# Kernel tuning notes

Hardware: AMD Instinct MI355X
Metric: run time of the kernel (lower is better)

Reference implementation:

```python
import jax, jax.numpy as jnp
import numpy as np

NUM_HEADS = 12
HEAD_DIM = 64
LOGIT_SCALE_MAX = 4.605170185988092  # log(1/0.01), open_clip default
EPS = 1e-12  # F.normalize eps


def setup_inputs() -> dict:
    key = jax.random.key(0)
    ks = jax.random.split(key, 8)
    N, L, C = 2, 2048, 768
    return {
        "x": jax.random.normal(ks[0], (N, L, C), dtype=jnp.float32),
        "in_proj_w": jax.random.normal(ks[1], (3 * C, C), dtype=jnp.float32) * 0.02,
        "in_proj_b": jax.random.normal(ks[2], (3 * C,), dtype=jnp.float32) * 0.02,
        "logit_scale": jax.random.normal(ks[3], (NUM_HEADS, 1, 1), dtype=jnp.float32),
        "learned_scale": jnp.ones((NUM_HEADS,), dtype=jnp.float32),
        "out_proj_w": jax.random.normal(ks[4], (C, C), dtype=jnp.float32) * 0.02,
        "out_proj_b": jax.random.normal(ks[5], (C,), dtype=jnp.float32) * 0.02,
        "attn_mask": jnp.zeros((L, L), dtype=jnp.float32),
    }


def _l2norm(t):
    # F.normalize(dim=-1): x / max(||x||, eps)
    n = jnp.linalg.norm(t, axis=-1, keepdims=True)
    return t / jnp.maximum(n, EPS)


def reference(x, in_proj_w, in_proj_b, logit_scale, learned_scale,
              out_proj_w, out_proj_b, attn_mask):
    N, L, C = x.shape
    H, D = NUM_HEADS, HEAD_DIM
    # packed QKV projection: [N, L, 3C]
    qkv = jnp.einsum("nlc,fc->nlf", x, in_proj_w) + in_proj_b
    q, k, v = jnp.split(qkv, 3, axis=-1)
    # [N, L, C] -> [N, H, L, D]
    to_heads = lambda t: t.reshape(N, L, H, D).transpose(0, 2, 1, 3)
    q, k, v = to_heads(q), to_heads(k), to_heads(v)
    # cosine attention with clamped exp logit scale per head
    attn = jnp.einsum("nhld,nhmd->nhlm", _l2norm(q), _l2norm(k))
    ls = jnp.exp(jnp.minimum(logit_scale, LOGIT_SCALE_MAX))  # [H,1,1]
    attn = attn * ls[None]  # broadcast over [N,H,L,L]
    attn = attn + attn_mask  # additive mask [L,L]
    attn = jax.nn.softmax(attn, axis=-1)
    out = jnp.einsum("nhlm,nhmd->nhld", attn, v)
    # learned per-head output scale
    out = out * learned_scale[None, :, None, None]
    # [N,H,L,D] -> [N,L,C]
    out = out.transpose(0, 2, 1, 3).reshape(N, L, C)
    out = jnp.einsum("nlc,fc->nlf", out, out_proj_w) + out_proj_b
    return out
```

## Files before the change

kernel.cpp:

```cpp
#include <hip/hip_runtime.h>
#include <math.h>

#define NB   2
#define SEQ  2048
#define CH   768
#define NH   12
#define HD   64
#define F3   2304
#define LSMAX 4.605170185988092f
#define LOG2E 1.4426950408889634f

typedef _Float16 f16;
typedef __attribute__((ext_vector_type(8))) _Float16 f16x8;
typedef __attribute__((ext_vector_type(4))) _Float16 f16x4;
typedef __attribute__((ext_vector_type(2))) _Float16 f16x2;
typedef __attribute__((ext_vector_type(4))) float f32x4;

#define QSZ   3145728
#define OATT  (3 * QSZ)
#define XHOFF 12582912
#define W1OFF 15728640
#define W2OFF 17498112
#define FLAGO 18087936

#define KP   72
#define VP   136
#define PPIT 76
#define GP   40

__global__ __launch_bounds__(256) void cvt_f16(const float* __restrict__ X,
                                               const float* __restrict__ W1,
                                               const float* __restrict__ W2,
                                               const float* __restrict__ M,
                                               f16* __restrict__ Xh,
                                               f16* __restrict__ W1h,
                                               f16* __restrict__ W2h,
                                               int* __restrict__ flag)
{
    int tid = blockIdx.x * 256 + threadIdx.x;
    if (blockIdx.y == 3) {
        if (tid < 1048576) {
            float4 v = ((const float4*)M)[tid];
            bool nz = (v.x != 0.f) || (v.y != 0.f) || (v.z != 0.f) || (v.w != 0.f);
            if (__any(nz) && (threadIdx.x & 63) == 0) atomicOr(flag, 1);
        }
        return;
    }
    const float* src; f16* dst; int n4;
    switch (blockIdx.y) {
        case 0:  src = X;  dst = Xh;  n4 = 786432;  break;
        case 1:  src = W1; dst = W1h; n4 = 442368;  break;
        default: src = W2; dst = W2h; n4 = 147456;  break;
    }
    if (tid < n4) {
        float4 v = ((const float4*)src)[tid];
        f16x4 o = {(f16)v.x, (f16)v.y, (f16)v.z, (f16)v.w};
        ((f16x4*)dst)[tid] = o;
    }
}

__global__ __launch_bounds__(256, 3) void qkv_gemm(const f16* __restrict__ Xh,
                                                   const f16* __restrict__ Wh,
                                                   const float* __restrict__ bias,
                                                   const float* __restrict__ logit_scale,
                                                   f16* __restrict__ qkv16)
{
    __shared__ f16 As[128 * GP];
    __shared__ f16 Bs[128 * GP];
    const int t    = threadIdx.x;
    const int w    = t >> 6;
    const int lane = t & 63;
    const int quad = lane >> 4;
    const int sub  = lane & 15;
    const int wm   = w & 1, wn = w >> 1;
    const int f0   = blockIdx.x * 128;
    const int m0   = blockIdx.y * 128;
    const int srow = t >> 1;
    const int sk   = (t & 1) * 16;

    const f16* ag = Xh + (size_t)(m0 + srow) * CH + sk;
    const f16* bg = Wh + (size_t)(f0 + srow) * CH + sk;
    f16x8 a0 = *(const f16x8*)(ag);
    f16x8 a1 = *(const f16x8*)(ag + 8);
    f16x8 b0 = *(const f16x8*)(bg);
    f16x8 b1 = *(const f16x8*)(bg + 8);

    f32x4 acc[4][4];
#pragma unroll
    for (int i = 0; i < 4; ++i)
#pragma unroll
        for (int j = 0; j < 4; ++j) acc[i][j] = (f32x4){0.f, 0.f, 0.f, 0.f};

    for (int k0 = 0; k0 < CH; k0 += 32) {
        __syncthreads();
        *(f16x8*)&As[srow * GP + sk + 0] = a0;
        *(f16x8*)&As[srow * GP + sk + 8] = a1;
        *(f16x8*)&Bs[srow * GP + sk + 0] = b0;
        *(f16x8*)&Bs[srow * GP + sk + 8] = b1;
        __syncthreads();
        if (k0 + 32 < CH) {
            a0 = *(const f16x8*)(ag + k0 + 32);
            a1 = *(const f16x8*)(ag + k0 + 40);
            b0 = *(const f16x8*)(bg + k0 + 32);
            b1 = *(const f16x8*)(bg + k0 + 40);
        }
        f16x8 af[4], bf[4];
#pragma unroll
        for (int i = 0; i < 4; ++i) {
            af[i] = *(const f16x8*)&As[(wm * 64 + i * 16 + sub) * GP + quad * 8];
            bf[i] = *(const f16x8*)&Bs[(wn * 64 + i * 16 + sub) * GP + quad * 8];
        }
#pragma unroll
        for (int i = 0; i < 4; ++i)
#pragma unroll
            for (int j = 0; j < 4; ++j)
                acc[i][j] = __builtin_amdgcn_mfma_f32_16x16x32_f16(af[i], bf[j], acc[i][j], 0, 0, 0);
    }

    const int t3 = f0 / CH;
    const int h  = ((f0 + wn * 64) % CH) >> 6;
    f16* dst = qkv16 + (size_t)t3 * QSZ;
    float lsv = (t3 == 0) ? __expf(fminf(logit_scale[h], LSMAX)) * LOG2E : 1.0f;
    float bb[4];
#pragma unroll
    for (int j = 0; j < 4; ++j) bb[j] = bias[f0 + wn * 64 + j * 16 + sub];
#pragma unroll
    for (int i = 0; i < 4; ++i) {
#pragma unroll
        for (int r = 0; r < 4; ++r) {
            int m = m0 + wm * 64 + i * 16 + quad * 4 + r;
            int n = m >> 11, l = m & 2047;
            float v[4];
#pragma unroll
            for (int j = 0; j < 4; ++j) v[j] = acc[i][j][r] + bb[j];
            float scale = 1.0f;
            if (t3 < 2) {
                float ss = v[0] * v[0] + v[1] * v[1] + v[2] * v[2] + v[3] * v[3];
#pragma unroll
                for (int mk = 1; mk < 16; mk <<= 1) ss += __shfl_xor(ss, mk, 64);
                scale = 1.0f / fmaxf(sqrtf(ss), 1e-12f);
                if (t3 == 0) scale *= lsv;
            }
            f16* drow = dst + (((size_t)n * NH + h) * SEQ + l) * HD;
#pragma unroll
            for (int j = 0; j < 4; ++j)
                drow[j * 16 + sub] = (f16)(v[j] * scale);
        }
    }
}

__global__ __launch_bounds__(256, 3) void attn(const f16* __restrict__ Qh,
                                               const f16* __restrict__ Kh,
                                               const f16* __restrict__ Vh,
                                               const float* __restrict__ M32,
                                               const float* __restrict__ lscale,
                                               const int* __restrict__ flag,
                                               f16* __restrict__ Og)
{
    __shared__ f16 Ks[128 * KP];
    __shared__ f16 Vt[64 * VP];
    __shared__ f16 QP[64 * PPIT];

    const int t    = threadIdx.x;
    const int w    = t >> 6;
    const int lane = t & 63;
    const int quad = lane >> 4;
    const int sub  = lane & 15;
    const int qb   = blockIdx.x * 64;
    const int h    = blockIdx.y, n = blockIdx.z;
    const bool has_mask = (*flag) != 0;

    const f16* Qg = Qh + ((size_t)(n * NH + h) * SEQ + qb) * HD;
    const f16* Kg = Kh + (size_t)(n * NH + h) * SEQ * HD;
    const f16* Vg = Vh + (size_t)(n * NH + h) * SEQ * HD;
    const float* Mg = M32 + (size_t)(qb + w * 16 + quad * 4) * SEQ;

#pragma unroll
    for (int rep = 0; rep < 2; ++rep) {
        int id = rep * 256 + t;
        int row = id >> 3, c8 = id & 7;
        f16x8 v = *(const f16x8*)&Qg[row * 64 + c8 * 8];
        *(f16x4*)&QP[row * PPIT + c8 * 8 + 0] = (f16x4){v[0], v[1], v[2], v[3]};
        *(f16x4*)&QP[row * PPIT + c8 * 8 + 4] = (f16x4){v[4], v[5], v[6], v[7]};
    }

    const int krow = t >> 1;
    const int kcb  = (t & 1) * 32;
    f16x8 kr0, kr1, kr2, kr3, vr0, vr1, vr2, vr3;
    {
        const f16* kp = Kg + krow * 64 + kcb;
        kr0 = *(const f16x8*)(kp + 0);
        kr1 = *(const f16x8*)(kp + 8);
        kr2 = *(const f16x8*)(kp + 16);
        kr3 = *(const f16x8*)(kp + 24);
        const f16* vp = Vg + (2 * lane) * 64 + w * 16;
        vr0 = *(const f16x8*)(vp + 0);
        vr1 = *(const f16x8*)(vp + 8);
        vr2 = *(const f16x8*)(vp + 64);
        vr3 = *(const f16x8*)(vp + 72);
    }

    __syncthreads();
    f16x8 qf0, qf1;
    {
        f16x4 l0 = *(const f16x4*)&QP[(w * 16 + sub) * PPIT + quad * 8];
        f16x4 l1 = *(const f16x4*)&QP[(w * 16 + sub) * PPIT + quad * 8 + 4];
        f16x4 l2 = *(const f16x4*)&QP[(w * 16 + sub) * PPIT + 32 + quad * 8];
        f16x4 l3 = *(const f16x4*)&QP[(w * 16 + sub) * PPIT + 32 + quad * 8 + 4];
        qf0 = (f16x8){l0[0], l0[1], l0[2], l0[3], l1[0], l1[1], l1[2], l1[3]};
        qf1 = (f16x8){l2[0], l2[1], l2[2], l2[3], l3[0], l3[1], l3[2], l3[3]};
    }

    {
        f16* kd = &Ks[krow * KP + kcb];
        *(f16x8*)(kd + 0)  = kr0;
        *(f16x8*)(kd + 8)  = kr1;
        *(f16x8*)(kd + 16) = kr2;
        *(f16x8*)(kd + 24) = kr3;
#pragma unroll
        for (int j = 0; j < 8; ++j) {
            *(f16x2*)&Vt[(w * 16 + j) * VP + 2 * lane]     = (f16x2){vr0[j], vr2[j]};
            *(f16x2*)&Vt[(w * 16 + 8 + j) * VP + 2 * lane] = (f16x2){vr1[j], vr3[j]};
        }
    }
    __syncthreads();

    const f16x8 ones = {(f16)1.f, (f16)1.f, (f16)1.f, (f16)1.f,
                        (f16)1.f, (f16)1.f, (f16)1.f, (f16)1.f};
    f32x4 o[4];
    f32x4 l_acc = (f32x4){0.f, 0.f, 0.f, 0.f};
    float m_run[4];
#pragma unroll
    for (int dt = 0; dt < 4; ++dt) o[dt] = (f32x4){0.f, 0.f, 0.f, 0.f};
#pragma unroll
    for (int r = 0; r < 4; ++r) m_run[r] = -1e30f;

    const int NITER = SEQ / 128;
    for (int c = 0; c < NITER; ++c) {
        const int c0 = c * 128;
        if (c + 1 < NITER) {
            const f16* kp = Kg + (c0 + 128 + krow) * 64 + kcb;
            kr0 = *(const f16x8*)(kp + 0);
            kr1 = *(const f16x8*)(kp + 8);
            kr2 = *(const f16x8*)(kp + 16);
            kr3 = *(const f16x8*)(kp + 24);
            const f16* vp = Vg + (c0 + 128 + 2 * lane) * 64 + w * 16;
            vr0 = *(const f16x8*)(vp + 0);
            vr1 = *(const f16x8*)(vp + 8);
            vr2 = *(const f16x8*)(vp + 64);
            vr3 = *(const f16x8*)(vp + 72);
        }

        f32x4 s[8];
#pragma unroll
        for (int ct = 0; ct < 8; ++ct) {
            f16x8 kf0 = *(const f16x8*)&Ks[(ct * 16 + sub) * KP + quad * 8];
            f16x8 kf1 = *(const f16x8*)&Ks[(ct * 16 + sub) * KP + 32 + quad * 8];
            f32x4 a = (f32x4){0.f, 0.f, 0.f, 0.f};
            a = __builtin_amdgcn_mfma_f32_16x16x32_f16(qf0, kf0, a, 0, 0, 0);
            a = __builtin_amdgcn_mfma_f32_16x16x32_f16(qf1, kf1, a, 0, 0, 0);
            s[ct] = a;
        }
        if (has_mask) {
#pragma unroll
            for (int ct = 0; ct < 8; ++ct)
#pragma unroll
                for (int r = 0; r < 4; ++r)
                    s[ct][r] += LOG2E * Mg[(size_t)r * SEQ + c0 + ct * 16 + sub];
        }
        float mnew[4];
#pragma unroll
        for (int r = 0; r < 4; ++r) {
            float a01 = fmaxf(s[0][r], s[1][r]), a23 = fmaxf(s[2][r], s[3][r]);
            float a45 = fmaxf(s[4][r], s[5][r]), a67 = fmaxf(s[6][r], s[7][r]);
            mnew[r] = fmaxf(fmaxf(fmaxf(a01, a23), fmaxf(a45, a67)), m_run[r]);
        }
        {
            union { f16x2 h; int i; } p0, p1, v0, v1;
            p0.h = (f16x2){(f16)mnew[0], (f16)mnew[1]};
            p1.h = (f16x2){(f16)mnew[2], (f16)mnew[3]};
#pragma unroll
            for (int mk = 1; mk < 16; mk <<= 1) {
                v0.i = __shfl_xor(p0.i, mk, 64);
                v1.i = __shfl_xor(p1.i, mk, 64);
                p0.h = __builtin_elementwise_max(p0.h, v0.h);
                p1.h = __builtin_elementwise_max(p1.h, v1.h);
            }
            mnew[0] = (float)p0.h[0]; mnew[1] = (float)p0.h[1];
            mnew[2] = (float)p1.h[0]; mnew[3] = (float)p1.h[1];
        }
        float alpha[4];
#pragma unroll
        for (int r = 0; r < 4; ++r) {
            alpha[r] = exp2f(m_run[r] - mnew[r]);
            m_run[r] = mnew[r];
        }
#pragma unroll
        for (int dt = 0; dt < 4; ++dt)
#pragma unroll
            for (int r = 0; r < 4; ++r) o[dt][r] *= alpha[r];
#pragma unroll
        for (int r = 0; r < 4; ++r) l_acc[r] *= alpha[r];

#pragma unroll
        for (int hf = 0; hf < 2; ++hf) {
#pragma unroll
            for (int ct = 0; ct < 4; ++ct)
#pragma unroll
                for (int r = 0; r < 4; ++r) {
                    float p = exp2f(s[hf * 4 + ct][r] - mnew[r]);
                    QP[(w * 16 + quad * 4 + r) * PPIT + ct * 16 + sub] = (f16)p;
                }
            f16x4 p00 = *(const f16x4*)&QP[(w * 16 + sub) * PPIT + quad * 8];
            f16x4 p01 = *(const f16x4*)&QP[(w * 16 + sub) * PPIT + quad * 8 + 4];
            f16x4 p10 = *(const f16x4*)&QP[(w * 16 + sub) * PPIT + 32 + quad * 8];
            f16x4 p11 = *(const f16x4*)&QP[(w * 16 + sub) * PPIT + 32 + quad * 8 + 4];
            f16x8 pf0 = {p00[0], p00[1], p00[2], p00[3], p01[0], p01[1], p01[2], p01[3]};
            f16x8 pf1 = {p10[0], p10[1], p10[2], p10[3], p11[0], p11[1], p11[2], p11[3]};
            l_acc = __builtin_amdgcn_mfma_f32_16x16x32_f16(pf0, ones, l_acc, 0, 0, 0);
            l_acc = __builtin_amdgcn_mfma_f32_16x16x32_f16(pf1, ones, l_acc, 0, 0, 0);
#pragma unroll
            for (int dt = 0; dt < 4; ++dt) {
                f16x8 vf0 = *(const f16x8*)&Vt[(dt * 16 + sub) * VP + hf * 64 + quad * 8];
                f16x8 vf1 = *(const f16x8*)&Vt[(dt * 16 + sub) * VP + hf * 64 + 32 + quad * 8];
                o[dt] = __builtin_amdgcn_mfma_f32_16x16x32_f16(pf0, vf0, o[dt], 0, 0, 0);
                o[dt] = __builtin_amdgcn_mfma_f32_16x16x32_f16(pf1, vf1, o[dt], 0, 0, 0);
            }
        }

        if (c + 1 < NITER) {
            __syncthreads();
            f16* kd = &Ks[krow * KP + kcb];
            *(f16x8*)(kd + 0)  = kr0;
            *(f16x8*)(kd + 8)  = kr1;
            *(f16x8*)(kd + 16) = kr2;
            *(f16x8*)(kd + 24) = kr3;
#pragma unroll
            for (int j = 0; j < 8; ++j) {
                *(f16x2*)&Vt[(w * 16 + j) * VP + 2 * lane]     = (f16x2){vr0[j], vr2[j]};
                *(f16x2*)&Vt[(w * 16 + 8 + j) * VP + 2 * lane] = (f16x2){vr1[j], vr3[j]};
            }
            __syncthreads();
        }
    }
    float lsc = lscale[h];
#pragma unroll
    for (int r = 0; r < 4; ++r) {
        float inv = lsc / l_acc[r];
        int q = qb + w * 16 + quad * 4 + r;
#pragma unroll
        for (int dt = 0; dt < 4; ++dt)
            Og[((size_t)n * SEQ + q) * CH + h * 64 + dt * 16 + sub] =
                (f16)(o[dt][r] * inv);
    }
}

__global__ __launch_bounds__(256, 3) void out_gemm(const f16* __restrict__ A,
                                                   const f16* __restrict__ Wh,
                                                   const float* __restrict__ bias,
                                                   float* __restrict__ out)
{
    __shared__ f16 As[128 * GP];
    __shared__ f16 Bs[128 * GP];
    const int t    = threadIdx.x;
    const int w    = t >> 6;
    const int lane = t & 63;
    const int quad = lane >> 4;
    const int sub  = lane & 15;
    const int wm   = w & 1, wn = w >> 1;
    const int f0   = blockIdx.x * 128;
    const int m0   = blockIdx.y * 128;
    const int srow = t >> 1;
    const int sk   = (t & 1) * 16;

    const f16* ag = A + (size_t)(m0 + srow) * CH + sk;
    const f16* bg = Wh + (size_t)(f0 + srow) * CH + sk;
    f16x8 a0 = *(const f16x8*)(ag);
    f16x8 a1 = *(const f16x8*)(ag + 8);
    f16x8 b0 = *(const f16x8*)(bg);
    f16x8 b1 = *(const f16x8*)(bg + 8);

    f32x4 acc[4][4];
#pragma unroll
    for (int i = 0; i < 4; ++i)
#pragma unroll
        for (int j = 0; j < 4; ++j) acc[i][j] = (f32x4){0.f, 0.f, 0.f, 0.f};

    for (int k0 = 0; k0 < CH; k0 += 32) {
        __syncthreads();
        *(f16x8*)&As[srow * GP + sk + 0] = a0;
        *(f16x8*)&As[srow * GP + sk + 8] = a1;
        *(f16x8*)&Bs[srow * GP + sk + 0] = b0;
        *(f16x8*)&Bs[srow * GP + sk + 8] = b1;
        __syncthreads();
        if (k0 + 32 < CH) {
            a0 = *(const f16x8*)(ag + k0 + 32);
            a1 = *(const f16x8*)(ag + k0 + 40);
            b0 = *(const f16x8*)(bg + k0 + 32);
            b1 = *(const f16x8*)(bg + k0 + 40);
        }
        f16x8 af[4], bf[4];
#pragma unroll
        for (int i = 0; i < 4; ++i) {
            af[i] = *(const f16x8*)&As[(wm * 64 + i * 16 + sub) * GP + quad * 8];
            bf[i] = *(const f16x8*)&Bs[(wn * 64 + i * 16 + sub) * GP + quad * 8];
        }
#pragma unroll
        for (int i = 0; i < 4; ++i)
#pragma unroll
            for (int j = 0; j < 4; ++j)
                acc[i][j] = __builtin_amdgcn_mfma_f32_16x16x32_f16(af[i], bf[j], acc[i][j], 0, 0, 0);
    }
    float bb[4];
#pragma unroll
    for (int j = 0; j < 4; ++j) bb[j] = bias[f0 + wn * 64 + j * 16 + sub];
#pragma unroll
    for (int i = 0; i < 4; ++i)
#pragma unroll
        for (int r = 0; r < 4; ++r) {
            int m = m0 + wm * 64 + i * 16 + quad * 4 + r;
            float* orow = out + (size_t)m * CH + f0 + wn * 64;
#pragma unroll
            for (int j = 0; j < 4; ++j)
                orow[j * 16 + sub] = acc[i][j][r] + bb[j];
        }
}

extern "C" void kernel_launch(void* const* d_in, const int* in_sizes, int n_in,
                              void* d_out, int out_size, void* d_ws, size_t ws_size,
                              hipStream_t stream) {
    const float* x    = (const float*)d_in[0];
    const float* w1   = (const float*)d_in[1];
    const float* b1   = (const float*)d_in[2];
    const float* ls   = (const float*)d_in[3];
    const float* lrn  = (const float*)d_in[4];
    const float* w2   = (const float*)d_in[5];
    const float* b2   = (const float*)d_in[6];
    const float* msk  = (const float*)d_in[7];
    f16*   ws16 = (f16*)d_ws;
    int*   flag = (int*)(ws16 + FLAGO);
    float* out  = (float*)d_out;

    (void)hipMemsetAsync(flag, 0, 4, stream);
    hipLaunchKernelGGL(cvt_f16, dim3(4096, 4), dim3(256), 0, stream,
                       x, w1, w2, msk,
                       ws16 + XHOFF, ws16 + W1OFF, ws16 + W2OFF, flag);
    hipLaunchKernelGGL(qkv_gemm, dim3(F3 / 128, (NB * SEQ) / 128), dim3(256), 0, stream,
                       ws16 + XHOFF, ws16 + W1OFF, b1, ls, ws16);
    hipLaunchKernelGGL(attn, dim3(SEQ / 64, NH, NB), dim3(256), 0, stream,
                       ws16, ws16 + QSZ, ws16 + 2 * QSZ, msk, lrn, flag,
                       ws16 + OATT);
    hipLaunchKernelGGL(out_gemm, dim3(CH / 128, (NB * SEQ) / 128), dim3(256), 0, stream,
                       ws16 + OATT, ws16 + W2OFF, b2, out);
}
```

Measured before the change: 212.0 us.

## Read K fragments directly from global and double-buffer V tile in LDS

Drops the K shared-memory tile. Each wave now loads its QK^T MFMA operands straight from global memory (L2-cached, shared across the four waves), and Q fragments are also read directly. V is double-buffered in LDS with a two-stage register prefetch, so one barrier per iteration replaces two. This cuts LDS traffic and synchronisation, but each wave now issues redundant global K loads and sits on their latency before the S MFMAs.

Result: slower. 263.4 us (+24.2%).

```diff
diff --git a/kernel.cpp b/kernel.cpp
--- a/kernel.cpp
+++ b/kernel.cpp
@@ -23,7 +23,6 @@
 #define W2OFF 17498112
 #define FLAGO 18087936
 
-#define KP   72
 #define VP   136
 #define PPIT 76
 #define GP   40
@@ -157,9 +156,8 @@
                                                const int* __restrict__ flag,
                                                f16* __restrict__ Og)
 {
-    __shared__ f16 Ks[128 * KP];
-    __shared__ f16 Vt[64 * VP];
-    __shared__ f16 QP[64 * PPIT];
+    __shared__ f16 Vt[2][64 * VP];
+    __shared__ f16 Ps[64 * PPIT];
 
     const int t    = threadIdx.x;
     const int w    = t >> 6;
@@ -175,53 +173,28 @@
     const f16* Vg = Vh + (size_t)(n * NH + h) * SEQ * HD;
     const float* Mg = M32 + (size_t)(qb + w * 16 + quad * 4) * SEQ;
 
-#pragma unroll
-    for (int rep = 0; rep < 2; ++rep) {
-        int id = rep * 256 + t;
-        int row = id >> 3, c8 = id & 7;
-        f16x8 v = *(const f16x8*)&Qg[row * 64 + c8 * 8];
-        *(f16x4*)&QP[row * PPIT + c8 * 8 + 0] = (f16x4){v[0], v[1], v[2], v[3]};
-        *(f16x4*)&QP[row * PPIT + c8 * 8 + 4] = (f16x4){v[4], v[5], v[6], v[7]};
-    }
-
-    const int krow = t >> 1;
-    const int kcb  = (t & 1) * 32;
-    f16x8 kr0, kr1, kr2, kr3, vr0, vr1, vr2, vr3;
+    f16x8 qf0 = *(const f16x8*)&Qg[(w * 16 + sub) * 64 + quad * 8];
+    f16x8 qf1 = *(const f16x8*)&Qg[(w * 16 + sub) * 64 + 32 + quad * 8];
+
+    f16x8 vr0, vr1, vr2, vr3;
     {
-        const f16* kp = Kg + krow * 64 + kcb;
-        kr0 = *(const f16x8*)(kp + 0);
-        kr1 = *(const f16x8*)(kp + 8);
-        kr2 = *(const f16x8*)(kp + 16);
-        kr3 = *(const f16x8*)(kp + 24);
         const f16* vp = Vg + (2 * lane) * 64 + w * 16;
         vr0 = *(const f16x8*)(vp + 0);
         vr1 = *(const f16x8*)(vp + 8);
         vr2 = *(const f16x8*)(vp + 64);
         vr3 = *(const f16x8*)(vp + 72);
     }
-
-    __syncthreads();
-    f16x8 qf0, qf1;
+#pragma unroll
+    for (int j = 0; j < 8; ++j) {
+        *(f16x2*)&Vt[0][(w * 16 + j) * VP + 2 * lane]     = (f16x2){vr0[j], vr2[j]};
+        *(f16x2*)&Vt[0][(w * 16 + 8 + j) * VP + 2 * lane] = (f16x2){vr1[j], vr3[j]};
+    }
     {
-        f16x4 l0 = *(const f16x4*)&QP[(w * 16 + sub) * PPIT + quad * 8];
-        f16x4 l1 = *(const f16x4*)&QP[(w * 16 + sub) * PPIT + quad * 8 + 4];
-        f16x4 l2 = *(const f16x4*)&QP[(w * 16 + sub) * PPIT + 32 + quad * 8];
-        f16x4 l3 = *(const f16x4*)&QP[(w * 16 + sub) * PPIT + 32 + quad * 8 + 4];
-        qf0 = (f16x8){l0[0], l0[1], l0[2], l0[3], l1[0], l1[1], l1[2], l1[3]};
-        qf1 = (f16x8){l2[0], l2[1], l2[2], l2[3], l3[0], l3[1], l3[2], l3[3]};
-    }
-
-    {
-        f16* kd = &Ks[krow * KP + kcb];
-        *(f16x8*)(kd + 0)  = kr0;
-        *(f16x8*)(kd + 8)  = kr1;
-        *(f16x8*)(kd + 16) = kr2;
-        *(f16x8*)(kd + 24) = kr3;
-#pragma unroll
-        for (int j = 0; j < 8; ++j) {
-            *(f16x2*)&Vt[(w * 16 + j) * VP + 2 * lane]     = (f16x2){vr0[j], vr2[j]};
-            *(f16x2*)&Vt[(w * 16 + 8 + j) * VP + 2 * lane] = (f16x2){vr1[j], vr3[j]};
-        }
+        const f16* vp = Vg + (128 + 2 * lane) * 64 + w * 16;
+        vr0 = *(const f16x8*)(vp + 0);
+        vr1 = *(const f16x8*)(vp + 8);
+        vr2 = *(const f16x8*)(vp + 64);
+        vr3 = *(const f16x8*)(vp + 72);
     }
     __syncthreads();
 
@@ -238,29 +211,43 @@
     const int NITER = SEQ / 128;
     for (int c = 0; c < NITER; ++c) {
         const int c0 = c * 128;
+        const int cur = c & 1, nxt = cur ^ 1;
+        if (c > 0) __syncthreads();
+
+        const f16* kbase = Kg + (size_t)c0 * 64;
+        f16x8 kf[8];
+#pragma unroll
+        for (int ct = 0; ct < 8; ++ct)
+            kf[ct] = *(const f16x8*)&kbase[(ct * 16 + sub) * 64 + quad * 8];
+
         if (c + 1 < NITER) {
-            const f16* kp = Kg + (c0 + 128 + krow) * 64 + kcb;
-            kr0 = *(const f16x8*)(kp + 0);
-            kr1 = *(const f16x8*)(kp + 8);
-            kr2 = *(const f16x8*)(kp + 16);
-            kr3 = *(const f16x8*)(kp + 24);
-            const f16* vp = Vg + (c0 + 128 + 2 * lane) * 64 + w * 16;
-            vr0 = *(const f16x8*)(vp + 0);
-            vr1 = *(const f16x8*)(vp + 8);
-            vr2 = *(const f16x8*)(vp + 64);
-            vr3 = *(const f16x8*)(vp + 72);
+#pragma unroll
+            for (int j = 0; j < 8; ++j) {
+                *(f16x2*)&Vt[nxt][(w * 16 + j) * VP + 2 * lane]     = (f16x2){vr0[j], vr2[j]};
+                *(f16x2*)&Vt[nxt][(w * 16 + 8 + j) * VP + 2 * lane] = (f16x2){vr1[j], vr3[j]};
+            }
+            if (c + 2 < NITER) {
+                const f16* vp = Vg + ((c + 2) * 128 + 2 * lane) * 64 + w * 16;
+                vr0 = *(const f16x8*)(vp + 0);
+                vr1 = *(const f16x8*)(vp + 8);
+                vr2 = *(const f16x8*)(vp + 64);
+                vr3 = *(const f16x8*)(vp + 72);
+            }
         }
 
         f32x4 s[8];
 #pragma unroll
         for (int ct = 0; ct < 8; ++ct) {
-            f16x8 kf0 = *(const f16x8*)&Ks[(ct * 16 + sub) * KP + quad * 8];
-            f16x8 kf1 = *(const f16x8*)&Ks[(ct * 16 + sub) * KP + 32 + quad * 8];
             f32x4 a = (f32x4){0.f, 0.f, 0.f, 0.f};
-            a = __builtin_amdgcn_mfma_f32_16x16x32_f16(qf0, kf0, a, 0, 0, 0);
-            a = __builtin_amdgcn_mfma_f32_16x16x32_f16(qf1, kf1, a, 0, 0, 0);
-            s[ct] = a;
-        }
+            s[ct] = __builtin_amdgcn_mfma_f32_16x16x32_f16(qf0, kf[ct], a, 0, 0, 0);
+        }
+#pragma unroll
+        for (int ct = 0; ct < 8; ++ct)
+            kf[ct] = *(const f16x8*)&kbase[(ct * 16 + sub) * 64 + 32 + quad * 8];
+#pragma unroll
+        for (int ct = 0; ct < 8; ++ct)
+            s[ct] = __builtin_amdgcn_mfma_f32_16x16x32_f16(qf1, kf[ct], s[ct], 0, 0, 0);
+
         if (has_mask) {
 #pragma unroll
             for (int ct = 0; ct < 8; ++ct)
@@ -309,38 +296,23 @@
 #pragma unroll
                 for (int r = 0; r < 4; ++r) {
                     float p = exp2f(s[hf * 4 + ct][r] - mnew[r]);
-                    QP[(w * 16 + quad * 4 + r) * PPIT + ct * 16 + sub] = (f16)p;
+                    Ps[(w * 16 + quad * 4 + r) * PPIT + ct * 16 + sub] = (f16)p;
                 }
-            f16x4 p00 = *(const f16x4*)&QP[(w * 16 + sub) * PPIT + quad * 8];
-            f16x4 p01 = *(const f16x4*)&QP[(w * 16 + sub) * PPIT + quad * 8 + 4];
-            f16x4 p10 = *(const f16x4*)&QP[(w * 16 + sub) * PPIT + 32 + quad * 8];
-            f16x4 p11 = *(const f16x4*)&QP[(w * 16 + sub) * PPIT + 32 + quad * 8 + 4];
+            f16x4 p00 = *(const f16x4*)&Ps[(w * 16 + sub) * PPIT + quad * 8];
+            f16x4 p01 = *(const f16x4*)&Ps[(w * 16 + sub) * PPIT + quad * 8 + 4];
+            f16x4 p10 = *(const f16x4*)&Ps[(w * 16 + sub) * PPIT + 32 + quad * 8];
+            f16x4 p11 = *(const f16x4*)&Ps[(w * 16 + sub) * PPIT + 32 + quad * 8 + 4];
             f16x8 pf0 = {p00[0], p00[1], p00[2], p00[3], p01[0], p01[1], p01[2], p01[3]};
             f16x8 pf1 = {p10[0], p10[1], p10[2], p10[3], p11[0], p11[1], p11[2], p11[3]};
             l_acc = __builtin_amdgcn_mfma_f32_16x16x32_f16(pf0, ones, l_acc, 0, 0, 0);
             l_acc = __builtin_amdgcn_mfma_f32_16x16x32_f16(pf1, ones, l_acc, 0, 0, 0);
 #pragma unroll
             for (int dt = 0; dt < 4; ++dt) {
-                f16x8 vf0 = *(const f16x8*)&Vt[(dt * 16 + sub) * VP + hf * 64 + quad * 8];
-                f16x8 vf1 = *(const f16x8*)&Vt[(dt * 16 + sub) * VP + hf * 64 + 32 + quad * 8];
+                f16x8 vf0 = *(const f16x8*)&Vt[cur][(dt * 16 + sub) * VP + hf * 64 + quad * 8];
+                f16x8 vf1 = *(const f16x8*)&Vt[cur][(dt * 16 + sub) * VP + hf * 64 + 32 + quad * 8];
                 o[dt] = __builtin_amdgcn_mfma_f32_16x16x32_f16(pf0, vf0, o[dt], 0, 0, 0);
                 o[dt] = __builtin_amdgcn_mfma_f32_16x16x32_f16(pf1, vf1, o[dt], 0, 0, 0);
             }
-        }
-
-        if (c + 1 < NITER) {
-            __syncthreads();
-            f16* kd = &Ks[krow * KP + kcb];
-            *(f16x8*)(kd + 0)  = kr0;
-            *(f16x8*)(kd + 8)  = kr1;
-            *(f16x8*)(kd + 16) = kr2;
-            *(f16x8*)(kd + 24) = kr3;
-#pragma unroll
-            for (int j = 0; j < 8; ++j) {
-                *(f16x2*)&Vt[(w * 16 + j) * VP + 2 * lane]     = (f16x2){vr0[j], vr2[j]};
-                *(f16x2*)&Vt[(w * 16 + 8 + j) * VP + 2 * lane] = (f16x2){vr1[j], vr3[j]};
-            }
-            __syncthreads();
         }
     }
     float lsc = lscale[h];
```
